# Performance work log

Measured on AMD Instinct MI355X. Metric: run time of the kernel, lower is better.

Reference implementation:

```python
import jax, jax.numpy as jnp
import numpy as np

B, H, L, N2 = 8, 256, 4096, 32  # N2 = d_state // 2 (conjugate-pair parameterization)


def _s4d_kernel(log_dt, log_A_real, A_imag, C_re, C_im, length):
    """S4D (diag) SSM convolution kernel via ZOH discretization. Returns (H, L) real."""
    dt = jnp.exp(log_dt)                               # (H,)
    A = -jnp.exp(log_A_real) + 1j * A_imag             # (H, N2) complex, Re<0
    C = C_re + 1j * C_im                               # (H, N2)
    dtA = A * dt[:, None]                              # (H, N2)
    # Vandermonde matrix exp(dtA * l), l = 0..L-1 : (H, N2, L)
    V = jnp.exp(dtA[:, :, None] * jnp.arange(length, dtype=log_dt.dtype))
    Ck = C * (jnp.exp(dtA) - 1.0) / A                  # absorb ZOH B-scaling into C
    # factor 2 accounts for the implicit conjugate pairs
    return 2.0 * jnp.einsum('hn,hnl->hl', Ck, V).real


def setup_inputs() -> dict:
    key = jax.random.key(0)
    ks = jax.random.split(key, 8)
    hidden_states = jax.random.normal(ks[0], (B, H, L), dtype=jnp.float32)
    # dt log-uniform in [1e-3, 1e-1]
    log_dt = jnp.log(1e-3) + jax.random.uniform(ks[1], (H,), dtype=jnp.float32) * (
        jnp.log(1e-1) - jnp.log(1e-3))
    # diag-lin init: A = -1/2 + i*pi*n
    log_A_real = jnp.log(0.5 * jnp.ones((H, N2), dtype=jnp.float32))
    A_imag = jnp.broadcast_to(np.pi * jnp.arange(N2, dtype=jnp.float32), (H, N2)).copy()
    C_re = jax.random.normal(ks[2], (H, N2), dtype=jnp.float32) * (0.5 ** 0.5)
    C_im = jax.random.normal(ks[3], (H, N2), dtype=jnp.float32) * (0.5 ** 0.5)
    D = jax.random.normal(ks[4], (H,), dtype=jnp.float32)
    # output position-wise linear H -> 2H followed by GLU
    W_out = jax.random.normal(ks[5], (2 * H, H), dtype=jnp.float32) * (1.0 / np.sqrt(H))
    b_out = jnp.zeros((2 * H,), dtype=jnp.float32)
    return {"hidden_states": hidden_states, "log_dt": log_dt, "log_A_real": log_A_real,
            "A_imag": A_imag, "C_re": C_re, "C_im": C_im, "D": D,
            "W_out": W_out, "b_out": b_out}


def reference(hidden_states, log_dt, log_A_real, A_imag, C_re, C_im, D, W_out, b_out):
    _, _, length = hidden_states.shape
    k = _s4d_kernel(log_dt, log_A_real, A_imag, C_re, C_im, length)  # (H, L)
    n_fft = 2 * length
    k_f = jnp.fft.rfft(k, n=n_fft)                     # (H, L+1)
    u_f = jnp.fft.rfft(hidden_states, n=n_fft)         # (B, H, L+1)
    y = jnp.fft.irfft(u_f * k_f, n=n_fft)[..., :length]  # causal long conv
    y = y + hidden_states * D[:, None]                 # skip connection
    y = jax.nn.gelu(y, approximate=False)              # torch F.gelu (exact erf)
    y = jnp.einsum('oh,bhl->bol', W_out, y) + b_out[None, :, None]  # (B, 2H, L)
    a, g = jnp.split(y, 2, axis=1)                     # GLU
    return a * jax.nn.sigmoid(g)                       # (B, H, L)
```

## Files before the change

kernel.cpp:

```cpp
#include <hip/hip_runtime.h>
#include <hip/hip_bf16.h>

#define B_   8
#define H_   256
#define L_   4096
#define N2_  32

typedef __attribute__((ext_vector_type(8))) short bf16x8;
typedef __attribute__((ext_vector_type(4))) float f32x4;

__device__ __forceinline__ unsigned short f2bf(float x) {
    __hip_bfloat16 h = __float2bfloat16(x);
    unsigned short us;
    __builtin_memcpy(&us, &h, 2);
    return us;
}

union BF8 { ushort4 u4[2]; unsigned short s[8]; bf16x8 v; };

__device__ __forceinline__ float gelu_exact(float y) {
    return 0.5f * y * (1.0f + erff(y * 0.70710678118654752440f));
}

__device__ __forceinline__ void fast_sincos(float x, float* s, float* c) {
    float rev = x * 0.15915494309189535f;
    rev = rev - floorf(rev);
    *s = __builtin_amdgcn_sinf(rev);
    *c = __builtin_amdgcn_cosf(rev);
}

__global__ __launch_bounds__(256) void prep_kernel(
    const float* __restrict__ log_dt,
    const float* __restrict__ log_A_real,
    const float* __restrict__ A_imag,
    const float* __restrict__ C_re,
    const float* __restrict__ C_im,
    const float* __restrict__ W,
    unsigned short* __restrict__ MAT,
    unsigned short* __restrict__ W2)
{
    const int bid = blockIdx.x;
    const int tid = threadIdx.x;
    if (bid >= 256) {
        int gq = (bid - 256) * 256 + tid;
        int m = gq >> 6, t = gq & 63;
        int ks = t >> 4, sub = t & 15;
        int gr = sub >> 1, e4 = (sub & 1) * 4;
        int klog = ks * 64 + ((gr ^ (m & 7)) << 3) + e4;
        float4 wv = *(const float4*)&W[m * 256 + klog];
        ushort4 o;
        o.x = f2bf(wv.x); o.y = f2bf(wv.y); o.z = f2bf(wv.z); o.w = f2bf(wv.w);
        *(ushort4*)&W2[ks * 32768 + m * 64 + gr * 8 + e4] = o;
        return;
    }
    const int h    = bid;
    const int j    = tid & 63;
    const int part = tid >> 6;

    __shared__ float sAr[32], sAi[32], sK2r[32], sK2i[32];
    __shared__ float sTap[4][64];
    __shared__ unsigned short sQ[64 * 68];

    unsigned short* __restrict__ Pd  = MAT + (size_t)h * 12288;
    unsigned short* __restrict__ Tkd = Pd + 4096;
    unsigned short* __restrict__ Qd  = Pd + 8192;
    const float dt = __expf(log_dt[h]);

    if (tid < 32) {
        int n = tid;
        float Ar = -__expf(log_A_real[h * 32 + n]);
        float Ai = A_imag[h * 32 + n];
        float er = __expf(dt * Ar);
        float s, c; fast_sincos(dt * Ai, &s, &c);
        float wr = er * c, wi = er * s;
        float Cr = C_re[h * 32 + n], Ci = C_im[h * 32 + n];
        float den = Ar * Ar + Ai * Ai;
        float nr = wr - 1.0f, ni = wi;
        float qr = (nr * Ar + ni * Ai) / den;
        float qi = (ni * Ar - nr * Ai) / den;
        sAr[n] = Ar; sAi[n] = Ai;
        sK2r[n] = 2.0f * (Cr * qr - Ci * qi);
        sK2i[n] = 2.0f * (Cr * qi + Ci * qr);
    }
    __syncthreads();

    {
        float pdt = dt * (float)(63 - j);
        #pragma unroll
        for (int q = 0; q < 8; ++q) {
            int n = part * 8 + q;
            float mag = __expf(pdt * sAr[n]);
            float s, c; fast_sincos(pdt * sAi[n], &s, &c);
            Pd[(2 * n)     * 64 + j] = f2bf(mag * c);
            Pd[(2 * n + 1) * 64 + j] = f2bf(mag * s);
        }
    }
    {
        float jdt = dt * (float)j;
        float acc = 0.0f;
        #pragma unroll
        for (int q = 0; q < 8; ++q) {
            int n = part * 8 + q;
            float mag = __expf(jdt * sAr[n]);
            float s, c; fast_sincos(jdt * sAi[n], &s, &c);
            acc = fmaf(sK2r[n], mag * c, fmaf(-sK2i[n], mag * s, acc));
        }
        sTap[part][j] = acc;
        float j1dt = dt * (float)(j + 1);
        #pragma unroll
        for (int q = 0; q < 8; ++q) {
            int n = part * 8 + q;
            float mag = __expf(j1dt * sAr[n]);
            float s, c; fast_sincos(j1dt * sAi[n], &s, &c);
            float wpr = mag * c, wpi = mag * s;
            sQ[j * 68 + 2 * n]     = f2bf(sK2r[n] * wpr - sK2i[n] * wpi);
            sQ[j * 68 + 2 * n + 1] = f2bf(-(sK2r[n] * wpi + sK2i[n] * wpr));
        }
    }
    __syncthreads();
    if (part == 0)
        sTap[0][j] = sTap[0][j] + sTap[1][j] + sTap[2][j] + sTap[3][j];
    __syncthreads();

    {
        int r  = tid >> 2;
        int c0 = (tid & 3) * 16;
        #pragma unroll
        for (int cc = 0; cc < 16; cc += 4) {
            int c = c0 + cc;
            ushort4 v;
            v.x = (r - c     >= 0) ? f2bf(sTap[0][r - c])     : (unsigned short)0;
            v.y = (r - c - 1 >= 0) ? f2bf(sTap[0][r - c - 1]) : (unsigned short)0;
            v.z = (r - c - 2 >= 0) ? f2bf(sTap[0][r - c - 2]) : (unsigned short)0;
            v.w = (r - c - 3 >= 0) ? f2bf(sTap[0][r - c - 3]) : (unsigned short)0;
            *(ushort4*)&Tkd[r * 64 + c] = v;
        }
    }
    #pragma unroll
    for (int it = 0; it < 4; ++it) {
        int quad = it * 256 + tid;
        int row = quad >> 4, c4 = (quad & 15) * 4;
        ushort4 v;
        v.x = sQ[row * 68 + c4];     v.y = sQ[row * 68 + c4 + 1];
        v.z = sQ[row * 68 + c4 + 2]; v.w = sQ[row * 68 + c4 + 3];
        *(ushort4*)&Qd[row * 64 + c4] = v;
    }
}

__global__ __launch_bounds__(256, 2) void s4_mfma_kernel(
    const float* __restrict__ u,
    const float* __restrict__ log_dt,
    const float* __restrict__ log_A_real,
    const float* __restrict__ A_imag,
    const float* __restrict__ Dp,
    const unsigned short* __restrict__ MAT,
    unsigned short* __restrict__ Gout)
{
    __shared__ __align__(16) unsigned char smem[4 * 17408];
    const int tid  = threadIdx.x;
    const int w    = tid >> 6;
    const int lane = tid & 63;
    const int ln15 = lane & 15;
    const int hi4  = (lane >> 4) * 4;
    const int hi8  = (lane >> 4) * 8;
    const int bid  = blockIdx.x;
    const int b    = bid >> 6, hg = bid & 63;
    const int h    = hg * 4 + w;

    float* Eb = (float*)(smem + w * 17408);
    unsigned short* yb = (unsigned short*)(smem + w * 17408);

    const float* __restrict__ urow = u + ((size_t)(b * H_ + h)) * L_;
    const unsigned short* __restrict__ Ph  = MAT + (size_t)h * 12288;
    const unsigned short* __restrict__ Tkh = Ph + 4096;
    const unsigned short* __restrict__ Qh  = Ph + 8192;

    float wTr, wTi;
    {
        int n = lane & 31;
        float dt = expf(log_dt[h]);
        float Ar = -expf(log_A_real[h * 32 + n]);
        float Ai = A_imag[h * 32 + n];
        float er = expf(dt * Ar); float s, c; sincosf(dt * Ai, &s, &c);
        float pr = er * c, pi = er * s;
        #pragma unroll
        for (int k = 0; k < 6; ++k) { float a2 = pr*pr - pi*pi, b2 = 2.0f*pr*pi; pr = a2; pi = b2; }
        wTr = pr; wTi = pi;
    }

    bf16x8 ufr[4][2];
    #pragma unroll
    for (int nt = 0; nt < 4; ++nt) {
        int c = nt * 16 + ln15;
        #pragma unroll
        for (int ks = 0; ks < 2; ++ks) {
            const float* p = urow + c * 64 + ks * 32 + hi8;
            float4 lo = *(const float4*)p;
            float4 hi = *(const float4*)(p + 4);
            BF8 t8;
            t8.s[0]=f2bf(lo.x); t8.s[1]=f2bf(lo.y); t8.s[2]=f2bf(lo.z); t8.s[3]=f2bf(lo.w);
            t8.s[4]=f2bf(hi.x); t8.s[5]=f2bf(hi.y); t8.s[6]=f2bf(hi.z); t8.s[7]=f2bf(hi.w);
            ufr[nt][ks] = t8.v;
        }
    }
    #pragma unroll
    for (int mt = 0; mt < 4; ++mt) {
        bf16x8 pa[2];
        #pragma unroll
        for (int ks = 0; ks < 2; ++ks)
            pa[ks] = *(const bf16x8*)&Ph[(mt * 16 + ln15) * 64 + ks * 32 + hi8];
        f32x4 e[4];
        #pragma unroll
        for (int nt = 0; nt < 4; ++nt) e[nt] = (f32x4){0.f, 0.f, 0.f, 0.f};
        #pragma unroll
        for (int ks = 0; ks < 2; ++ks)
            #pragma unroll
            for (int nt = 0; nt < 4; ++nt)
                e[nt] = __builtin_amdgcn_mfma_f32_16x16x32_bf16(pa[ks], ufr[nt][ks], e[nt], 0, 0, 0);
        #pragma unroll
        for (int nt = 0; nt < 4; ++nt)
            *(f32x4*)&Eb[(nt * 16 + ln15) * 68 + mt * 16 + hi4] = e[nt];
    }
    __syncthreads();

    if (lane < 32) {
        int n2 = 2 * lane;
        float Xr = 0.0f, Xi = 0.0f;
        float2 e = *(float2*)&Eb[n2];
        #pragma unroll 4
        for (int c = 0; c < 64; ++c) {
            float2 en = e;
            if (c < 63) en = *(float2*)&Eb[(c + 1) * 68 + n2];
            *(float2*)&Eb[c * 68 + n2] = make_float2(Xr, Xi);
            float nXr = fmaf(wTr, Xr, fmaf(-wTi, Xi, e.x));
            float nXi = fmaf(wTi, Xr, fmaf( wTr, Xi, e.y));
            Xr = nXr; Xi = nXi; e = en;
        }
    }
    __syncthreads();

    bf16x8 sfr[4][2];
    #pragma unroll
    for (int nt = 0; nt < 4; ++nt) {
        int c = nt * 16 + ln15;
        #pragma unroll
        for (int ks = 0; ks < 2; ++ks) {
            float4 lo = *(const float4*)&Eb[c * 68 + ks * 32 + hi8];
            float4 hi = *(const float4*)&Eb[c * 68 + ks * 32 + hi8 + 4];
            BF8 t8;
            t8.s[0]=f2bf(lo.x); t8.s[1]=f2bf(lo.y); t8.s[2]=f2bf(lo.z); t8.s[3]=f2bf(lo.w);
            t8.s[4]=f2bf(hi.x); t8.s[5]=f2bf(hi.y); t8.s[6]=f2bf(hi.z); t8.s[7]=f2bf(hi.w);
            sfr[nt][ks] = t8.v;
        }
    }
    const float Dh = Dp[h];
    #pragma unroll
    for (int mt = 0; mt < 4; ++mt) {
        bf16x8 ta[2], qa[2];
        #pragma unroll
        for (int ks = 0; ks < 2; ++ks) {
            ta[ks] = *(const bf16x8*)&Tkh[(mt * 16 + ln15) * 64 + ks * 32 + hi8];
            qa[ks] = *(const bf16x8*)&Qh [(mt * 16 + ln15) * 64 + ks * 32 + hi8];
        }
        #pragma unroll
        for (int nt = 0; nt < 4; ++nt) {
            f32x4 a = (f32x4){0.f, 0.f, 0.f, 0.f};
            #pragma unroll
            for (int ks = 0; ks < 2; ++ks) {
                a = __builtin_amdgcn_mfma_f32_16x16x32_bf16(ta[ks], ufr[nt][ks], a, 0, 0, 0);
                a = __builtin_amdgcn_mfma_f32_16x16x32_bf16(qa[ks], sfr[nt][ks], a, 0, 0, 0);
            }
            int c  = nt * 16 + ln15;
            int j0 = mt * 16 + hi4;
            float4 uu = *(const float4*)&urow[c * 64 + j0];
            ushort4 o;
            o.x = f2bf(gelu_exact(a[0] + Dh * uu.x));
            o.y = f2bf(gelu_exact(a[1] + Dh * uu.y));
            o.z = f2bf(gelu_exact(a[2] + Dh * uu.z));
            o.w = f2bf(gelu_exact(a[3] + Dh * uu.w));
            *(ushort4*)&yb[c * 68 + j0] = o;
        }
    }
    __syncthreads();

    unsigned short* __restrict__ Grow = Gout + ((size_t)(b * 64 + hg)) * (L_ * 4);
    #pragma unroll
    for (int it = 0; it < 16; ++it) {
        int l = it * 256 + tid;
        int c = l >> 6, j = l & 63;
        ushort4 pk;
        pk.x = ((unsigned short*)(smem + 0 * 17408))[c * 68 + j];
        pk.y = ((unsigned short*)(smem + 1 * 17408))[c * 68 + j];
        pk.z = ((unsigned short*)(smem + 2 * 17408))[c * 68 + j];
        pk.w = ((unsigned short*)(smem + 3 * 17408))[c * 68 + j];
        *(ushort4*)&Grow[(size_t)l * 4] = pk;
    }
}

__global__ __launch_bounds__(256, 4) void glu_gemm_kernel(
    const unsigned short* __restrict__ G,
    const unsigned short* __restrict__ W2,
    const float* __restrict__ bo,
    float* __restrict__ out)
{
    __shared__ __align__(16) unsigned char smem[36864];
    unsigned short* sW = (unsigned short*)smem;

    const int tid  = threadIdx.x;
    const int lane = tid & 63;
    const int wv   = tid >> 6;
    const int wm   = wv >> 1;
    const int wn   = wv & 1;
    const int ln15 = lane & 15;
    const int hi   = lane >> 4;

    const int l0 = blockIdx.x * 64;
    const int m0 = blockIdx.y * 128;
    const int b  = blockIdx.z;
    const int col0 = l0 + wn * 32 + ln15;

    f32x4 acc[8][2];
    #pragma unroll
    for (int i = 0; i < 8; ++i)
        #pragma unroll
        for (int j = 0; j < 2; ++j) acc[i][j] = (f32x4){0.f, 0.f, 0.f, 0.f};

    BF8 bb[2][2];
    auto loadB = [&](int ksub, BF8* dst) {
        int hg0 = ksub * 8 + hi * 2;
        size_t base = ((size_t)(b * 64 + hg0) * 4096 + col0) * 4;
        dst[0].u4[0] = *(const ushort4*)&G[base];
        dst[0].u4[1] = *(const ushort4*)&G[base + 16384];
        dst[1].u4[0] = *(const ushort4*)&G[base + 64];
        dst[1].u4[1] = *(const ushort4*)&G[base + 16384 + 64];
    };
    loadB(0, bb[0]);

    for (int ksub = 0; ksub < 8; ++ksub) {
        if ((ksub & 1) == 0) {
            const int ks = ksub >> 1;
            __syncthreads();
            const unsigned short* src1 = W2 + (size_t)ks * 32768 + m0 * 64;
            const unsigned short* src2 = W2 + (size_t)ks * 32768 + (256 + m0) * 64;
            uint4 t[8];
            #pragma unroll
            for (int i = 0; i < 4; ++i) t[i]     = *(const uint4*)&src1[i * 2048 + tid * 8];
            #pragma unroll
            for (int i = 0; i < 4; ++i) t[4 + i] = *(const uint4*)&src2[i * 2048 + tid * 8];
            #pragma unroll
            for (int i = 0; i < 8; ++i)
                *(uint4*)&sW[i * 2048 + tid * 8] = t[i];
            __syncthreads();
        }
        if (ksub < 7) loadB(ksub + 1, bb[(ksub + 1) & 1]);
        const BF8* bc = bb[ksub & 1];
        const int gl = (ksub & 1) * 4 + hi;
        #pragma unroll
        for (int half = 0; half < 2; ++half) {
            bf16x8 af[4];
            #pragma unroll
            for (int mt = 0; mt < 4; ++mt) {
                int r = half * 128 + wm * 64 + mt * 16 + ln15;
                af[mt] = *(const bf16x8*)((const unsigned char*)sW + r * 128 + ((gl ^ (r & 7)) << 4));
            }
            #pragma unroll
            for (int mt = 0; mt < 4; ++mt)
                #pragma unroll
                for (int nb = 0; nb < 2; ++nb)
                    acc[half * 4 + mt][nb] =
                        __builtin_amdgcn_mfma_f32_16x16x32_bf16(af[mt], bc[nb].v,
                                                                acc[half * 4 + mt][nb], 0, 0, 0);
        }
    }

    __syncthreads();
    float* sEp = (float*)smem + wv * 2304;
    #pragma unroll
    for (int mt = 0; mt < 4; ++mt) {
        int r0 = mt * 16 + hi * 4;
        float4 ba = *(const float4*)&bo[m0 + wm * 64 + r0];
        float4 bg = *(const float4*)&bo[256 + m0 + wm * 64 + r0];
        #pragma unroll
        for (int nb = 0; nb < 2; ++nb) {
            #pragma unroll
            for (int rr = 0; rr < 4; ++rr) {
                float a = acc[mt][nb][rr]     + ((const float*)&ba)[rr];
                float g = acc[4 + mt][nb][rr] + ((const float*)&bg)[rr];
                sEp[(r0 + rr) * 36 + nb * 16 + ln15] = a / (1.0f + expf(-g));
            }
        }
    }
    __syncthreads();
    {
        const int rl = lane >> 3;
        const int c4 = (lane & 7) * 4;
        float* obase = out + ((size_t)(b * 256 + m0 + wm * 64)) * 4096 + l0 + wn * 32;
        #pragma unroll
        for (int ps = 0; ps < 8; ++ps) {
            int row = ps * 8 + rl;
            float4 v = *(const float4*)&sEp[row * 36 + c4];
            *(float4*)&obase[(size_t)row * 4096 + c4] = v;
        }
    }
}

extern "C" void kernel_launch(void* const* d_in, const int* in_sizes, int n_in,
                              void* d_out, int out_size, void* d_ws, size_t ws_size,
                              hipStream_t stream) {
    (void)in_sizes; (void)n_in; (void)out_size;
    const float* hs     = (const float*)d_in[0];
    const float* log_dt = (const float*)d_in[1];
    const float* logA   = (const float*)d_in[2];
    const float* Aim    = (const float*)d_in[3];
    const float* Cre    = (const float*)d_in[4];
    const float* Cim    = (const float*)d_in[5];
    const float* Dp     = (const float*)d_in[6];
    const float* Wout   = (const float*)d_in[7];
    const float* bout   = (const float*)d_in[8];
    float* out          = (float*)d_out;

    unsigned short* G   = (unsigned short*)d_ws;
    unsigned short* MAT = (unsigned short*)((char*)d_ws + 16777216);
    unsigned short* W2  = (unsigned short*)((char*)d_ws + 23068672);

    if (ws_size < (size_t)23330816) return;

    prep_kernel<<<dim3(384), dim3(256), 0, stream>>>(
        log_dt, logA, Aim, Cre, Cim, Wout, MAT, W2);
    s4_mfma_kernel<<<dim3(512), dim3(256), 0, stream>>>(
        hs, log_dt, logA, Aim, Dp, MAT, G);
    glu_gemm_kernel<<<dim3(64, 2, 8), dim3(256), 0, stream>>>(
        G, W2, bout, out);
}
```

Baseline: 57.47 us.

## Fold D skip into conv tap, retile G layout, stage G tile in LDS

Folds the D skip term into tap 0 of the causal conv matrix, so the S4 kernel no longer reloads u in its epilogue. Changes the intermediate G layout so each 64-column L tile across all H is contiguous. The GLU GEMM then loads that tile into LDS once and loops over both output halves (M passes) inside one block, halving the grid and not rereading G per half. It also prefetches W stages into registers across iterations. The cost is more LDS per block, lower occupancy (launch bounds 2), and the D term now being rounded to bf16.

```diff
diff --git a/kernel.cpp b/kernel.cpp
--- a/kernel.cpp
+++ b/kernel.cpp
@@ -35,6 +35,7 @@
     const float* __restrict__ A_imag,
     const float* __restrict__ C_re,
     const float* __restrict__ C_im,
+    const float* __restrict__ Dp,
     const float* __restrict__ W,
     unsigned short* __restrict__ MAT,
     unsigned short* __restrict__ W2)
@@ -118,8 +119,11 @@
         }
     }
     __syncthreads();
-    if (part == 0)
-        sTap[0][j] = sTap[0][j] + sTap[1][j] + sTap[2][j] + sTap[3][j];
+    if (part == 0) {
+        float v = sTap[0][j] + sTap[1][j] + sTap[2][j] + sTap[3][j];
+        if (j == 0) v += Dp[h];
+        sTap[0][j] = v;
+    }
     __syncthreads();
 
     {
@@ -152,7 +156,6 @@
     const float* __restrict__ log_dt,
     const float* __restrict__ log_A_real,
     const float* __restrict__ A_imag,
-    const float* __restrict__ Dp,
     const unsigned short* __restrict__ MAT,
     unsigned short* __restrict__ Gout)
 {
@@ -253,7 +256,6 @@
             sfr[nt][ks] = t8.v;
         }
     }
-    const float Dh = Dp[h];
     #pragma unroll
     for (int mt = 0; mt < 4; ++mt) {
         bf16x8 ta[2], qa[2];
@@ -272,18 +274,17 @@
             }
             int c  = nt * 16 + ln15;
             int j0 = mt * 16 + hi4;
-            float4 uu = *(const float4*)&urow[c * 64 + j0];
             ushort4 o;
-            o.x = f2bf(gelu_exact(a[0] + Dh * uu.x));
-            o.y = f2bf(gelu_exact(a[1] + Dh * uu.y));
-            o.z = f2bf(gelu_exact(a[2] + Dh * uu.z));
-            o.w = f2bf(gelu_exact(a[3] + Dh * uu.w));
+            o.x = f2bf(gelu_exact(a[0]));
+            o.y = f2bf(gelu_exact(a[1]));
+            o.z = f2bf(gelu_exact(a[2]));
+            o.w = f2bf(gelu_exact(a[3]));
             *(ushort4*)&yb[c * 68 + j0] = o;
         }
     }
     __syncthreads();
 
-    unsigned short* __restrict__ Grow = Gout + ((size_t)(b * 64 + hg)) * (L_ * 4);
+    unsigned short* __restrict__ Gbase = Gout + ((size_t)b << 20);
     #pragma unroll
     for (int it = 0; it < 16; ++it) {
         int l = it * 256 + tid;
@@ -293,18 +294,18 @@
         pk.y = ((unsigned short*)(smem + 1 * 17408))[c * 68 + j];
         pk.z = ((unsigned short*)(smem + 2 * 17408))[c * 68 + j];
         pk.w = ((unsigned short*)(smem + 3 * 17408))[c * 68 + j];
-        *(ushort4*)&Grow[(size_t)l * 4] = pk;
-    }
-}
-
-__global__ __launch_bounds__(256, 4) void glu_gemm_kernel(
+        *(ushort4*)&Gbase[((size_t)(c * 64 + hg)) * 256 + j * 4] = pk;
+    }
+}
+
+__global__ __launch_bounds__(256, 2) void glu_gemm_kernel(
     const unsigned short* __restrict__ G,
     const unsigned short* __restrict__ W2,
     const float* __restrict__ bo,
     float* __restrict__ out)
 {
-    __shared__ __align__(16) unsigned char smem[36864];
-    unsigned short* sW = (unsigned short*)smem;
+    __shared__ __align__(16) unsigned short sG[16384];
+    __shared__ __align__(16) unsigned short sW[16384];
 
     const int tid  = threadIdx.x;
     const int lane = tid & 63;
@@ -314,10 +315,33 @@
     const int ln15 = lane & 15;
     const int hi   = lane >> 4;
 
-    const int l0 = blockIdx.x * 64;
-    const int m0 = blockIdx.y * 128;
-    const int b  = blockIdx.z;
-    const int col0 = l0 + wn * 32 + ln15;
+    const int l6 = blockIdx.x;
+    const int b  = blockIdx.y;
+    const int l0 = l6 * 64;
+
+    const unsigned short* gsrc = G + ((size_t)(b * 64 + l6) << 14);
+    uint4 rg[8];
+    #pragma unroll
+    for (int i = 0; i < 8; ++i)
+        rg[i] = *(const uint4*)&gsrc[i * 2048 + tid * 8];
+
+    uint4 t[8];
+    auto stageW_issue = [&](int st) {
+        int pass = st >> 2, ks = st & 3, m0 = pass * 128;
+        const unsigned short* src1 = W2 + (size_t)ks * 32768 + m0 * 64;
+        const unsigned short* src2 = W2 + (size_t)ks * 32768 + (256 + m0) * 64;
+        #pragma unroll
+        for (int i = 0; i < 4; ++i) t[i]     = *(const uint4*)&src1[i * 2048 + tid * 8];
+        #pragma unroll
+        for (int i = 0; i < 4; ++i) t[4 + i] = *(const uint4*)&src2[i * 2048 + tid * 8];
+    };
+    stageW_issue(0);
+
+    #pragma unroll
+    for (int i = 0; i < 8; ++i) *(uint4*)&sG[i * 2048 + tid * 8] = rg[i];
+    #pragma unroll
+    for (int i = 0; i < 8; ++i) *(uint4*)&sW[i * 2048 + tid * 8] = t[i];
+    __syncthreads();
 
     f32x4 acc[8][2];
     #pragma unroll
@@ -325,81 +349,80 @@
         #pragma unroll
         for (int j = 0; j < 2; ++j) acc[i][j] = (f32x4){0.f, 0.f, 0.f, 0.f};
 
-    BF8 bb[2][2];
-    auto loadB = [&](int ksub, BF8* dst) {
-        int hg0 = ksub * 8 + hi * 2;
-        size_t base = ((size_t)(b * 64 + hg0) * 4096 + col0) * 4;
-        dst[0].u4[0] = *(const ushort4*)&G[base];
-        dst[0].u4[1] = *(const ushort4*)&G[base + 16384];
-        dst[1].u4[0] = *(const ushort4*)&G[base + 64];
-        dst[1].u4[1] = *(const ushort4*)&G[base + 16384 + 64];
-    };
-    loadB(0, bb[0]);
-
-    for (int ksub = 0; ksub < 8; ++ksub) {
-        if ((ksub & 1) == 0) {
-            const int ks = ksub >> 1;
-            __syncthreads();
-            const unsigned short* src1 = W2 + (size_t)ks * 32768 + m0 * 64;
-            const unsigned short* src2 = W2 + (size_t)ks * 32768 + (256 + m0) * 64;
-            uint4 t[8];
-            #pragma unroll
-            for (int i = 0; i < 4; ++i) t[i]     = *(const uint4*)&src1[i * 2048 + tid * 8];
-            #pragma unroll
-            for (int i = 0; i < 4; ++i) t[4 + i] = *(const uint4*)&src2[i * 2048 + tid * 8];
-            #pragma unroll
-            for (int i = 0; i < 8; ++i)
-                *(uint4*)&sW[i * 2048 + tid * 8] = t[i];
-            __syncthreads();
-        }
-        if (ksub < 7) loadB(ksub + 1, bb[(ksub + 1) & 1]);
-        const BF8* bc = bb[ksub & 1];
-        const int gl = (ksub & 1) * 4 + hi;
-        #pragma unroll
-        for (int half = 0; half < 2; ++half) {
-            bf16x8 af[4];
+    for (int st = 0; st < 8; ++st) {
+        const int pass = st >> 2, ks = st & 3;
+        if (st < 7) stageW_issue(st + 1);
+
+        #pragma unroll
+        for (int k2 = 0; k2 < 2; ++k2) {
+            const int ksub = ks * 2 + k2;
+            BF8 bfr[2];
+            #pragma unroll
+            for (int nb = 0; nb < 2; ++nb) {
+                int col = wn * 32 + nb * 16 + ln15;
+                int hg0 = ksub * 8 + hi * 2;
+                bfr[nb].u4[0] = *(const ushort4*)&sG[(hg0 * 64 + col) * 4];
+                bfr[nb].u4[1] = *(const ushort4*)&sG[((hg0 + 1) * 64 + col) * 4];
+            }
+            const int gl = k2 * 4 + hi;
+            #pragma unroll
+            for (int half = 0; half < 2; ++half) {
+                #pragma unroll
+                for (int mt = 0; mt < 4; ++mt) {
+                    int r = half * 128 + wm * 64 + mt * 16 + ln15;
+                    bf16x8 af = *(const bf16x8*)((const unsigned char*)sW + r * 128 +
+                                                 ((gl ^ (r & 7)) << 4));
+                    #pragma unroll
+                    for (int nb = 0; nb < 2; ++nb)
+                        acc[half * 4 + mt][nb] =
+                            __builtin_amdgcn_mfma_f32_16x16x32_bf16(af, bfr[nb].v,
+                                                                    acc[half * 4 + mt][nb], 0, 0, 0);
+                }
+            }
+        }
+        __syncthreads();
+
+        if (ks == 3) {
+            const int m0 = pass * 128;
+            float* sEp = (float*)sW + wv * 2048;
             #pragma unroll
             for (int mt = 0; mt < 4; ++mt) {
-                int r = half * 128 + wm * 64 + mt * 16 + ln15;
-                af[mt] = *(const bf16x8*)((const unsigned char*)sW + r * 128 + ((gl ^ (r & 7)) << 4));
-            }
-            #pragma unroll
-            for (int mt = 0; mt < 4; ++mt)
+                int r0 = mt * 16 + hi * 4;
+                float4 ba = *(const float4*)&bo[m0 + wm * 64 + r0];
+                float4 bg = *(const float4*)&bo[256 + m0 + wm * 64 + r0];
                 #pragma unroll
                 for (int nb = 0; nb < 2; ++nb)
-                    acc[half * 4 + mt][nb] =
-                        __builtin_amdgcn_mfma_f32_16x16x32_bf16(af[mt], bc[nb].v,
-                                                                acc[half * 4 + mt][nb], 0, 0, 0);
-        }
-    }
-
-    __syncthreads();
-    float* sEp = (float*)smem + wv * 2304;
-    #pragma unroll
-    for (int mt = 0; mt < 4; ++mt) {
-        int r0 = mt * 16 + hi * 4;
-        float4 ba = *(const float4*)&bo[m0 + wm * 64 + r0];
-        float4 bg = *(const float4*)&bo[256 + m0 + wm * 64 + r0];
-        #pragma unroll
-        for (int nb = 0; nb < 2; ++nb) {
-            #pragma unroll
-            for (int rr = 0; rr < 4; ++rr) {
-                float a = acc[mt][nb][rr]     + ((const float*)&ba)[rr];
-                float g = acc[4 + mt][nb][rr] + ((const float*)&bg)[rr];
-                sEp[(r0 + rr) * 36 + nb * 16 + ln15] = a / (1.0f + expf(-g));
-            }
-        }
-    }
-    __syncthreads();
-    {
-        const int rl = lane >> 3;
-        const int c4 = (lane & 7) * 4;
-        float* obase = out + ((size_t)(b * 256 + m0 + wm * 64)) * 4096 + l0 + wn * 32;
-        #pragma unroll
-        for (int ps = 0; ps < 8; ++ps) {
-            int row = ps * 8 + rl;
-            float4 v = *(const float4*)&sEp[row * 36 + c4];
-            *(float4*)&obase[(size_t)row * 4096 + c4] = v;
+                    #pragma unroll
+                    for (int rr = 0; rr < 4; ++rr) {
+                        float a = acc[mt][nb][rr]     + ((const float*)&ba)[rr];
+                        float g = acc[4 + mt][nb][rr] + ((const float*)&bg)[rr];
+                        sEp[(r0 + rr) * 32 + nb * 16 + ln15] = a / (1.0f + __expf(-g));
+                    }
+            }
+            __syncthreads();
+            {
+                const int rl = lane >> 3, c4 = (lane & 7) * 4;
+                const float* sEpr = (const float*)sW + wv * 2048;
+                float* obase = out + ((size_t)(b * 256 + m0 + wm * 64)) * 4096 + l0 + wn * 32;
+                #pragma unroll
+                for (int ps = 0; ps < 8; ++ps) {
+                    int row = ps * 8 + rl;
+                    float4 v = *(const float4*)&sEpr[row * 32 + c4];
+                    *(float4*)&obase[(size_t)row * 4096 + c4] = v;
+                }
+            }
+            if (st < 7) {
+                #pragma unroll
+                for (int i = 0; i < 8; ++i)
+                    #pragma unroll
+                    for (int j = 0; j < 2; ++j) acc[i][j] = (f32x4){0.f, 0.f, 0.f, 0.f};
+                __syncthreads();
+            }
+        }
+        if (st < 7) {
+            #pragma unroll
+            for (int i = 0; i < 8; ++i) *(uint4*)&sW[i * 2048 + tid * 8] = t[i];
+            __syncthreads();
         }
     }
 }
@@ -426,9 +449,9 @@
     if (ws_size < (size_t)23330816) return;
 
     prep_kernel<<<dim3(384), dim3(256), 0, stream>>>(
-        log_dt, logA, Aim, Cre, Cim, Wout, MAT, W2);
+        log_dt, logA, Aim, Cre, Cim, Dp, Wout, MAT, W2);
     s4_mfma_kernel<<<dim3(512), dim3(256), 0, stream>>>(
-        hs, log_dt, logA, Aim, Dp, MAT, G);
-    glu_gemm_kernel<<<dim3(64, 2, 8), dim3(256), 0, stream>>>(
+        hs, log_dt, logA, Aim, MAT, G);
+    glu_gemm_kernel<<<dim3(64, 8), dim3(256), 0, stream>>>(
         G, W2, bout, out);
 }
```

New measurement: 83.08 us. 44.6% more time.
